# Performance work log

Hardware: AMD Instinct MI355X
Metric: run time of the kernel (lower is better)

Reference implementation:

```python
import jax, jax.numpy as jnp
import numpy as np

N_Q = 24
MEAS = (2, 5, 10, 18, 21)


def _build_gates():
    # encoding layer: RY(edge[i]) on wire i
    g = [("ry", "e", i, i) for i in range(N_Q)]
    spec = [
        ("ry", 0, 0), ("ry", 1, 1), ("cx", 0, 1),
        ("ry", 2, 2), ("ry", 3, 3), ("cx", 3, 2),
        ("ry", 4, 4), ("ry", 5, 5), ("cx", 4, 5),
        ("ry", 6, 6), ("ry", 7, 7), ("cx", 7, 6),
        ("ry", 8, 8), ("ry", 9, 9), ("cx", 8, 9),
        ("ry", 10, 10), ("ry", 11, 11), ("cx", 11, 10),
        ("ry", 12, 12), ("ry", 13, 13), ("cx", 12, 13),
        ("ry", 14, 14), ("ry", 15, 15), ("cx", 15, 14),
        ("ry", 16, 16), ("ry", 17, 17), ("cx", 16, 17),
        ("ry", 18, 18), ("ry", 19, 19), ("cx", 19, 18),
        ("ry", 20, 20), ("ry", 21, 21), ("cx", 20, 21),
        ("ry", 22, 22), ("ry", 23, 23), ("cx", 23, 22),
        ("ry", 24, 1), ("ry", 25, 2), ("cx", 1, 2),
        ("ry", 26, 5), ("ry", 27, 6), ("cx", 6, 5),
        ("ry", 28, 9), ("ry", 29, 10), ("cx", 9, 10),
        ("ry", 30, 13), ("ry", 31, 14), ("cx", 14, 13),
        ("ry", 32, 17), ("ry", 33, 18), ("cx", 17, 18),
        ("ry", 34, 21), ("ry", 35, 22), ("cx", 22, 21),
        ("ry", 36, 2), ("ry", 37, 5), ("cx", 2, 5),
        ("ry", 38, 10), ("ry", 39, 13), ("cx", 13, 10),
        ("ry", 40, 18), ("ry", 41, 21), ("cx", 21, 18),
        ("ry", 42, 5), ("ry", 43, 10), ("cx", 5, 10),
        ("ry", 44, 10), ("ry", 45, 18), ("cx", 10, 18),
        ("ry", 46, 5), ("ry", 47, 10), ("cx", 10, 5),
        ("ry", 48, 18), ("ry", 49, 21), ("cx", 18, 21),
        ("ry", 50, 2), ("ry", 51, 5), ("cx", 5, 2),
        ("ry", 52, 2), ("ry", 53, 5), ("ry", 54, 10), ("ry", 55, 18), ("ry", 56, 21),
    ]
    for op in spec:
        if op[0] == "ry":
            g.append(("ry", "t", op[1], op[2]))
        else:
            g.append(("cx", op[1], op[2]))
    return g


GATES = _build_gates()


def _ry(state, ang, w):
    # RY(ang) = [[cos(a/2), -sin(a/2)], [sin(a/2), cos(a/2)]] (real)
    h = 0.5 * ang
    c, s = jnp.cos(h), jnp.sin(h)
    U = jnp.stack([jnp.stack([c, -s]), jnp.stack([s, c])])
    return jnp.moveaxis(jnp.tensordot(U, state, axes=((1,), (w,))), 0, w)


def _cx(state, c, t):
    s = jnp.moveaxis(state, (c, t), (0, 1))
    s = jnp.stack([s[0], s[1][::-1]])  # flip target where control == 1
    return jnp.moveaxis(s, (0, 1), (c, t))


def _expz(state, w):
    p = jnp.moveaxis(state * state, w, 0)
    return jnp.sum(p[0]) - jnp.sum(p[1])


def _run(edge, theta):
    state = jnp.zeros((2,) * N_Q, jnp.float32).at[(0,) * N_Q].set(1.0)
    for g in GATES:
        if g[0] == "ry":
            ang = edge[g[2]] if g[1] == "e" else theta[g[2]]
            state = _ry(state, ang, g[3])
        else:
            state = _cx(state, g[1], g[2])
    return state


def _node_out(edge, theta):
    st = _run(edge, theta)
    ev = jnp.stack([_expz(st, w) for w in MEAS])
    return jnp.pi * (1.0 - ev)  # 2*pi*(1 - ev)/2


def setup_inputs() -> dict:
    key = jax.random.key(0)
    k0, k1, k2, k3, k4 = jax.random.split(key, 5)
    N, E, D = 4, 16, 8
    X = jax.random.uniform(k0, (N, D), jnp.float32)
    e = jax.random.uniform(k1, (E,), jnp.float32)
    Ri = jax.random.uniform(k2, (N, E), jnp.float32)
    Ro = jax.random.uniform(k3, (N, E), jnp.float32)
    theta = jax.random.uniform(k4, (57,), jnp.float32, 0.0, 2.0 * np.pi)
    return {"X": X, "e": e, "Ri": Ri, "Ro": Ro, "theta": theta}


def reference(X, e, Ri, Ro, theta):
    bo = Ro.T @ X                     # [E, D]
    bi = Ri.T @ X                     # [E, D]
    Rwo = Ro * e                      # edge-weighted incidence, e broadcasts over E
    Rwi = Ri * e
    mi = Rwi @ bo                     # [N, D]
    mo = Rwo @ bi                     # [N, D]
    M = jnp.concatenate([mi, mo, X], axis=1)  # [N, 24] angles per node
    return jax.vmap(_node_out, in_axes=(0, None))(M, theta)  # [N, 5]
```

## Files before the change

### kernel.cpp

```cpp
#include <hip/hip_runtime.h>
#include <math.h>


__device__ __forceinline__ void ry_dm(float& a, float& b, float& d, float c, float s) {
    float na = c*c*a - 2.0f*c*s*b + s*s*d;
    float nb = c*s*(a - d) + (c*c - s*s)*b;
    float nd = s*s*a + 2.0f*c*s*b + c*c*d;
    a = na; b = nb; d = nd;
}

template<int MASK>
__device__ __forceinline__ void apply_ry(float* amp, float c, float s) {
#pragma unroll
    for (int i = 0; i < 32; ++i) {
        if (!(i & MASK)) {
            float x = amp[i], y = amp[i | MASK];
            amp[i]        = c * x - s * y;
            amp[i | MASK] = s * x + c * y;
        }
    }
}

template<int MC, int MT>
__device__ __forceinline__ void apply_cx(float* amp) {
#pragma unroll
    for (int i = 0; i < 32; ++i) {
        if ((i & MC) && !(i & MT)) {
            float tmp = amp[i];
            amp[i] = amp[i | MT];
            amp[i | MT] = tmp;
        }
    }
}

__global__ __launch_bounds__(64) void nodenet_branch_kernel(
    const float* __restrict__ X, const float* __restrict__ e,
    const float* __restrict__ Ri, const float* __restrict__ Ro,
    const float* __restrict__ th, float* __restrict__ out)
{
    const int t    = threadIdx.x;
    const int node = blockIdx.x * 2 + (t >> 5);
    const int lig  = t & 31;
    const int base = t & 32;

    float Mv;
    {
        const int w    = lig & 15;
        const int half = lig >> 4;
        const int dcol = w & 7;
        const float* Aouter = (w < 8) ? Ri : Ro;
        const float* Ainner = (w < 8) ? Ro : Ri;
        const float x0 = X[0*8 + dcol], x1 = X[1*8 + dcol],
                    x2 = X[2*8 + dcol], x3 = X[3*8 + dcol];
        float acc = 0.0f;
        const int E0 = half * 8;
#pragma unroll
        for (int E = 0; E < 8; ++E) {
            const int Ei = E0 + E;
            float bsum = Ainner[0*16 + Ei]*x0 + Ainner[1*16 + Ei]*x1
                       + Ainner[2*16 + Ei]*x2 + Ainner[3*16 + Ei]*x3;
            acc += Aouter[node*16 + Ei] * e[Ei] * bsum;
        }
        acc += __shfl_xor(acc, 16);
        Mv = (lig < 16) ? acc : X[node*8 + ((lig - 16) & 7)];
    }

    float gs, gc;
    {
        const int id = (lig < 21) ? lig : 0;
        __sincosf(0.5f * th[36 + id], &gs, &gc);
    }

    const int ss = (lig < 6) ? lig : 0;
    const int Q   = ss==0?2 : ss==1?5 : ss==2?10 : ss==3?13 : ss==4?18 : 21;
    const int P   = ss==0?3 : ss==1?4 : ss==2?11 : ss==3?12 : ss==4?19 : 20;
    const int C   = ss==0?1 : ss==1?6 : ss==2?9  : ss==3?14 : ss==4?17 : 22;
    const int PC  = ss==0?0 : ss==1?7 : ss==2?8  : ss==3?15 : ss==4?16 : 23;
    const int tq2 = ss==0?25: ss==1?26: ss==2?29 : ss==3?30 : ss==4?33 : 34;
    const int tc2 = ss==0?24: ss==1?27: ss==2?28 : ss==3?31 : ss==4?32 : 35;

    const float mq  = __shfl(Mv, base + Q);
    const float mp  = __shfl(Mv, base + P);
    const float mc  = __shfl(Mv, base + C);
    const float mpc = __shfl(Mv, base + PC);

    float ra, rb, rd;
    {
        float sq, cq, sp, cp;
        __sincosf(0.5f*(mq + th[Q]), &sq, &cq);
        __sincosf(0.5f*(mp + th[P]), &sp, &cp);
        float aq = cp*cp*cq*cq + sp*sp*sq*sq;
        float bq = cq*sq;
        float dq = 1.0f - aq;

        float sc, cc, spc, cpc;
        __sincosf(0.5f*(mc + th[C]), &sc, &cc);
        __sincosf(0.5f*(mpc + th[PC]), &spc, &cpc);
        float ac = cpc*cpc*cc*cc + spc*spc*sc*sc;
        float bc = cc*sc;
        float dc = 1.0f - ac;

        float s2, c2;
        __sincosf(0.5f*th[tc2], &s2, &c2);
        float p0 = c2*c2*ac - 2.0f*c2*s2*bc + s2*s2*dc;

        float s1, c1;
        __sincosf(0.5f*th[tq2], &s1, &c1);
        ry_dm(aq, bq, dq, c1, s1);
        ra = p0*aq + (1.0f - p0)*dq;
        rb = bq;
        rd = p0*dq + (1.0f - p0)*aq;
    }

    {
        const float c38 = __shfl(gc, base + 2), s38 = __shfl(gs, base + 2);
        const float c39 = __shfl(gc, base + 3), s39 = __shfl(gs, base + 3);
        const float a3 = __shfl(ra, base + 3);
        const float b3 = __shfl(rb, base + 3);
        const float d3 = __shfl(rd, base + 3);
        float a = ra, b = rb, d = rd;
        ry_dm(a, b, d, c38, s38);
        float p0 = c39*c39*a3 - 2.0f*c39*s39*b3 + s39*s39*d3;
        float fa = p0*a + (1.0f - p0)*d;
        float fd = p0*d + (1.0f - p0)*a;
        if (lig == 2) { ra = fa; rb = b; rd = fd; }
    }

    float cph, sph, lam0;
    {
        float ad = ra - rd;
        float r  = sqrtf(ad*ad + 4.0f*rb*rb);
        lam0 = 0.5f * (1.0f + r);
        float c2p = (r > 1e-12f) ? ad / r : 1.0f;
        float s2p = (r > 1e-12f) ? 2.0f*rb / r : 0.0f;
        cph = sqrtf(fmaxf(0.0f, 0.5f*(1.0f + c2p)));
        sph = copysignf(sqrtf(fmaxf(0.0f, 0.5f*(1.0f - c2p))), s2p);
    }

    float u0[5], u1[5];
    float wgt = 1.0f;
    {
        const int slotOf[5] = {0, 1, 2, 4, 5};
#pragma unroll
        for (int b = 0; b < 5; ++b) {
            const float cb = __shfl(cph,  base + slotOf[b]);
            const float sb = __shfl(sph,  base + slotOf[b]);
            const float lb = __shfl(lam0, base + slotOf[b]);
            const int bit = (lig >> b) & 1;
            u0[b] = bit ? -sb : cb;
            u1[b] = bit ?  cb : sb;
            wgt  *= bit ? (1.0f - lb) : lb;
        }
    }

    float c_, s_;
#define BC(id) do { c_ = __shfl(gc, base + (id)); s_ = __shfl(gs, base + (id)); } while (0)

    BC(0); float v00 = c_*u0[0] - s_*u1[0], v01 = s_*u0[0] + c_*u1[0];
    BC(1); float v10 = c_*u0[1] - s_*u1[1], v11 = s_*u0[1] + c_*u1[1];
    float q01_0 = v00*v10, q01_1 = v01*v11, q01_2 = v00*v11, q01_3 = v01*v10;

    BC(4); float v30 = c_*u0[3] - s_*u1[3], v31 = s_*u0[3] + c_*u1[3];
    BC(5); float v40 = c_*u0[4] - s_*u1[4], v41 = s_*u0[4] + c_*u1[4];
    float q34_0 = v30*v40, q34_1 = v31*v40, q34_2 = v31*v41, q34_3 = v30*v41;

    BC(6);
    { float x = q01_0, y = q01_2; q01_0 = c_*x - s_*y; q01_2 = s_*x + c_*y;
      x = q01_1; y = q01_3;       q01_1 = c_*x - s_*y; q01_3 = s_*x + c_*y; }
    BC(7); float v20 = c_*u0[2] - s_*u1[2], v21 = s_*u0[2] + c_*u1[2];
    float q012[8];
    q012[0] = q01_0*v20; q012[1] = q01_1*v20; q012[2] = q01_2*v21; q012[3] = q01_3*v21;
    q012[4] = q01_0*v21; q012[5] = q01_1*v21; q012[6] = q01_2*v20; q012[7] = q01_3*v20;

    BC(8);
#pragma unroll
    for (int j = 0; j < 4; ++j) {
        float x = q012[j], y = q012[j + 4];
        q012[j] = c_*x - s_*y; q012[j + 4] = s_*x + c_*y;
    }
    BC(10);
    { float x, y;
      x = q012[0]; y = q012[2]; q012[0] = c_*x - s_*y; q012[2] = s_*x + c_*y;
      x = q012[1]; y = q012[3]; q012[1] = c_*x - s_*y; q012[3] = s_*x + c_*y;
      x = q012[4]; y = q012[6]; q012[4] = c_*x - s_*y; q012[6] = s_*x + c_*y;
      x = q012[5]; y = q012[7]; q012[5] = c_*x - s_*y; q012[7] = s_*x + c_*y; }

    BC(9);
    { float x = q34_0, y = q34_1; q34_0 = c_*x - s_*y; q34_1 = s_*x + c_*y;
      x = q34_2; y = q34_3;       q34_2 = c_*x - s_*y; q34_3 = s_*x + c_*y; }
    BC(13);
    { float x = q34_0, y = q34_2; q34_0 = c_*x - s_*y; q34_2 = s_*x + c_*y;
      x = q34_1; y = q34_3;       q34_1 = c_*x - s_*y; q34_3 = s_*x + c_*y; }

    float q34a[4] = {q34_0, q34_1, q34_2, q34_3};
    float amp[32];
#pragma unroll
    for (int j = 0; j < 32; ++j) {
        const int i2 = (j >> 2) & 1, i3 = (j >> 3) & 1, i4 = (j >> 4) & 1;
        amp[j] = q012[j & 7] * q34a[(i3 ^ i2) + 2*i4];
    }

    BC(11); apply_ry<4>(amp, c_, s_);
    apply_cx<4, 2>(amp);
    BC(12); apply_ry<8>(amp, c_, s_);
    apply_cx<8, 16>(amp);
    BC(14); apply_ry<1>(amp, c_, s_);
    BC(15); apply_ry<2>(amp, c_, s_);
    apply_cx<2, 1>(amp);

    float p[32];
#pragma unroll
    for (int j = 0; j < 32; ++j) p[j] = amp[j] * amp[j];

    float z0 = 0.f, z1 = 0.f, z2 = 0.f, z3 = 0.f, z4;
    float s0[16];
#pragma unroll
    for (int i = 0; i < 16; ++i) { s0[i] = p[2*i] + p[2*i+1]; z0 += p[2*i] - p[2*i+1]; }
    float s1v[8];
#pragma unroll
    for (int i = 0; i < 8; ++i)  { s1v[i] = s0[2*i] + s0[2*i+1]; z1 += s0[2*i] - s0[2*i+1]; }
    float s2v[4];
#pragma unroll
    for (int i = 0; i < 4; ++i)  { s2v[i] = s1v[2*i] + s1v[2*i+1]; z2 += s1v[2*i] - s1v[2*i+1]; }
    float s3v[2];
#pragma unroll
    for (int i = 0; i < 2; ++i)  { s3v[i] = s2v[2*i] + s2v[2*i+1]; z3 += s2v[2*i] - s2v[2*i+1]; }
    z4 = s3v[0] - s3v[1];
    const float zv[5] = {z0, z1, z2, z3, z4};

    float xv[5];
#pragma unroll
    for (int b = 0; b < 5; ++b) {
        const int m = 1 << b;
        float acc = 0.0f;
#pragma unroll
        for (int i = 0; i < 32; ++i)
            if (!(i & m)) acc += amp[i] * amp[i | m];
        xv[b] = 2.0f * acc;
    }

    float ev[5];
#pragma unroll
    for (int b = 0; b < 5; ++b) {
        BC(16 + b);
        ev[b] = wgt * ((c_*c_ - s_*s_) * zv[b] - 2.0f*c_*s_ * xv[b]);
    }
#undef BC

#pragma unroll
    for (int off = 1; off < 32; off <<= 1) {
#pragma unroll
        for (int b = 0; b < 5; ++b) ev[b] += __shfl_xor(ev[b], off);
    }

    if (lig < 5) {
        const float v = lig==0 ? ev[0] : lig==1 ? ev[1] : lig==2 ? ev[2]
                      : lig==3 ? ev[3] : ev[4];
        out[node*5 + lig] = 3.14159265358979f * (1.0f - v);
    }
}

extern "C" void kernel_launch(void* const* d_in, const int* in_sizes, int n_in,
                              void* d_out, int out_size, void* d_ws, size_t ws_size,
                              hipStream_t stream) {
    const float* X  = (const float*)d_in[0];
    const float* e  = (const float*)d_in[1];
    const float* Ri = (const float*)d_in[2];
    const float* Ro = (const float*)d_in[3];
    const float* th = (const float*)d_in[4];
    float* out = (float*)d_out;

    nodenet_branch_kernel<<<2, 64, 0, stream>>>(X, e, Ri, Ro, th, out);
}
```

Measured before the change: 9.585 us.

## Split each node's 32-amplitude state across two half-wavefronts, one node per block

Each node now gets a full 64-lane block, and the qubit-4 index is distributed across the two 32-lane halves. Every lane holds 16 amplitudes instead of 32. Gates that touch that bit become cross-half shuffles, and the launch grows from 2 to 4 blocks. The aim is to halve the per-thread serial arithmetic and register pressure on this latency-bound kernel, at the cost of extra cross-lane shuffles and a longer reduction.

```diff
diff --git a/kernel.cpp b/kernel.cpp
--- a/kernel.cpp
+++ b/kernel.cpp
@@ -10,25 +10,13 @@
 }
 
 template<int MASK>
-__device__ __forceinline__ void apply_ry(float* amp, float c, float s) {
-#pragma unroll
-    for (int i = 0; i < 32; ++i) {
+__device__ __forceinline__ void apply_ry16(float* amp, float c, float s) {
+#pragma unroll
+    for (int i = 0; i < 16; ++i) {
         if (!(i & MASK)) {
             float x = amp[i], y = amp[i | MASK];
             amp[i]        = c * x - s * y;
             amp[i | MASK] = s * x + c * y;
-        }
-    }
-}
-
-template<int MC, int MT>
-__device__ __forceinline__ void apply_cx(float* amp) {
-#pragma unroll
-    for (int i = 0; i < 32; ++i) {
-        if ((i & MC) && !(i & MT)) {
-            float tmp = amp[i];
-            amp[i] = amp[i | MT];
-            amp[i | MT] = tmp;
         }
     }
 }
@@ -39,17 +27,16 @@
     const float* __restrict__ th, float* __restrict__ out)
 {
     const int t    = threadIdx.x;
-    const int node = blockIdx.x * 2 + (t >> 5);
+    const int node = blockIdx.x;
     const int lig  = t & 31;
-    const int base = t & 32;
+    const int half = t >> 5;
 
     float Mv;
     {
-        const int w    = lig & 15;
-        const int half = lig >> 4;
+        const int w    = lig;
         const int dcol = w & 7;
-        const float* Aouter = (w < 8) ? Ri : Ro;
-        const float* Ainner = (w < 8) ? Ro : Ri;
+        const float* Aouter = ((w & 8) == 0) ? Ri : Ro;
+        const float* Ainner = ((w & 8) == 0) ? Ro : Ri;
         const float x0 = X[0*8 + dcol], x1 = X[1*8 + dcol],
                     x2 = X[2*8 + dcol], x3 = X[3*8 + dcol];
         float acc = 0.0f;
@@ -61,7 +48,7 @@
                        + Ainner[2*16 + Ei]*x2 + Ainner[3*16 + Ei]*x3;
             acc += Aouter[node*16 + Ei] * e[Ei] * bsum;
         }
-        acc += __shfl_xor(acc, 16);
+        acc += __shfl_xor(acc, 32);
         Mv = (lig < 16) ? acc : X[node*8 + ((lig - 16) & 7)];
     }
 
@@ -79,10 +66,10 @@
     const int tq2 = ss==0?25: ss==1?26: ss==2?29 : ss==3?30 : ss==4?33 : 34;
     const int tc2 = ss==0?24: ss==1?27: ss==2?28 : ss==3?31 : ss==4?32 : 35;
 
-    const float mq  = __shfl(Mv, base + Q);
-    const float mp  = __shfl(Mv, base + P);
-    const float mc  = __shfl(Mv, base + C);
-    const float mpc = __shfl(Mv, base + PC);
+    const float mq  = __shfl(Mv, Q);
+    const float mp  = __shfl(Mv, P);
+    const float mc  = __shfl(Mv, C);
+    const float mpc = __shfl(Mv, PC);
 
     float ra, rb, rd;
     {
@@ -113,11 +100,11 @@
     }
 
     {
-        const float c38 = __shfl(gc, base + 2), s38 = __shfl(gs, base + 2);
-        const float c39 = __shfl(gc, base + 3), s39 = __shfl(gs, base + 3);
-        const float a3 = __shfl(ra, base + 3);
-        const float b3 = __shfl(rb, base + 3);
-        const float d3 = __shfl(rd, base + 3);
+        const float c38 = __shfl(gc, 2), s38 = __shfl(gs, 2);
+        const float c39 = __shfl(gc, 3), s39 = __shfl(gs, 3);
+        const float a3 = __shfl(ra, 3);
+        const float b3 = __shfl(rb, 3);
+        const float d3 = __shfl(rd, 3);
         float a = ra, b = rb, d = rd;
         ry_dm(a, b, d, c38, s38);
         float p0 = c39*c39*a3 - 2.0f*c39*s39*b3 + s39*s39*d3;
@@ -143,9 +130,9 @@
         const int slotOf[5] = {0, 1, 2, 4, 5};
 #pragma unroll
         for (int b = 0; b < 5; ++b) {
-            const float cb = __shfl(cph,  base + slotOf[b]);
-            const float sb = __shfl(sph,  base + slotOf[b]);
-            const float lb = __shfl(lam0, base + slotOf[b]);
+            const float cb = __shfl(cph,  slotOf[b]);
+            const float sb = __shfl(sph,  slotOf[b]);
+            const float lb = __shfl(lam0, slotOf[b]);
             const int bit = (lig >> b) & 1;
             u0[b] = bit ? -sb : cb;
             u1[b] = bit ?  cb : sb;
@@ -154,15 +141,11 @@
     }
 
     float c_, s_;
-#define BC(id) do { c_ = __shfl(gc, base + (id)); s_ = __shfl(gs, base + (id)); } while (0)
+#define BC(id) do { c_ = __shfl(gc, (id)); s_ = __shfl(gs, (id)); } while (0)
 
     BC(0); float v00 = c_*u0[0] - s_*u1[0], v01 = s_*u0[0] + c_*u1[0];
     BC(1); float v10 = c_*u0[1] - s_*u1[1], v11 = s_*u0[1] + c_*u1[1];
     float q01_0 = v00*v10, q01_1 = v01*v11, q01_2 = v00*v11, q01_3 = v01*v10;
-
-    BC(4); float v30 = c_*u0[3] - s_*u1[3], v31 = s_*u0[3] + c_*u1[3];
-    BC(5); float v40 = c_*u0[4] - s_*u1[4], v41 = s_*u0[4] + c_*u1[4];
-    float q34_0 = v30*v40, q34_1 = v31*v40, q34_2 = v31*v41, q34_3 = v30*v41;
 
     BC(6);
     { float x = q01_0, y = q01_2; q01_0 = c_*x - s_*y; q01_2 = s_*x + c_*y;
@@ -184,59 +167,85 @@
       x = q012[1]; y = q012[3]; q012[1] = c_*x - s_*y; q012[3] = s_*x + c_*y;
       x = q012[4]; y = q012[6]; q012[4] = c_*x - s_*y; q012[6] = s_*x + c_*y;
       x = q012[5]; y = q012[7]; q012[5] = c_*x - s_*y; q012[7] = s_*x + c_*y; }
-
+    BC(14);
+    { float x, y;
+      x = q012[0]; y = q012[1]; q012[0] = c_*x - s_*y; q012[1] = s_*x + c_*y;
+      x = q012[2]; y = q012[3]; q012[2] = c_*x - s_*y; q012[3] = s_*x + c_*y;
+      x = q012[4]; y = q012[5]; q012[4] = c_*x - s_*y; q012[5] = s_*x + c_*y;
+      x = q012[6]; y = q012[7]; q012[6] = c_*x - s_*y; q012[7] = s_*x + c_*y; }
+
+    BC(4); float v30 = c_*u0[3] - s_*u1[3], v31 = s_*u0[3] + c_*u1[3];
+    BC(5); float v4h = half ? (s_*u0[4] + c_*u1[4]) : (c_*u0[4] - s_*u1[4]);
+    float qA = (half ? v31 : v30) * v4h;
+    float qB = (half ? v30 : v31) * v4h;
     BC(9);
-    { float x = q34_0, y = q34_1; q34_0 = c_*x - s_*y; q34_1 = s_*x + c_*y;
-      x = q34_2; y = q34_3;       q34_2 = c_*x - s_*y; q34_3 = s_*x + c_*y; }
+    { float x = qA, y = qB; qA = c_*x - s_*y; qB = s_*x + c_*y; }
     BC(13);
-    { float x = q34_0, y = q34_2; q34_0 = c_*x - s_*y; q34_2 = s_*x + c_*y;
-      x = q34_1; y = q34_3;       q34_1 = c_*x - s_*y; q34_3 = s_*x + c_*y; }
-
-    float q34a[4] = {q34_0, q34_1, q34_2, q34_3};
-    float amp[32];
-#pragma unroll
-    for (int j = 0; j < 32; ++j) {
-        const int i2 = (j >> 2) & 1, i3 = (j >> 3) & 1, i4 = (j >> 4) & 1;
-        amp[j] = q012[j & 7] * q34a[(i3 ^ i2) + 2*i4];
-    }
-
-    BC(11); apply_ry<4>(amp, c_, s_);
-    apply_cx<4, 2>(amp);
-    BC(12); apply_ry<8>(amp, c_, s_);
-    apply_cx<8, 16>(amp);
-    BC(14); apply_ry<1>(amp, c_, s_);
-    BC(15); apply_ry<2>(amp, c_, s_);
-    apply_cx<2, 1>(amp);
-
-    float p[32];
-#pragma unroll
-    for (int j = 0; j < 32; ++j) p[j] = amp[j] * amp[j];
-
-    float z0 = 0.f, z1 = 0.f, z2 = 0.f, z3 = 0.f, z4;
-    float s0[16];
-#pragma unroll
-    for (int i = 0; i < 16; ++i) { s0[i] = p[2*i] + p[2*i+1]; z0 += p[2*i] - p[2*i+1]; }
-    float s1v[8];
-#pragma unroll
-    for (int i = 0; i < 8; ++i)  { s1v[i] = s0[2*i] + s0[2*i+1]; z1 += s0[2*i] - s0[2*i+1]; }
-    float s2v[4];
-#pragma unroll
-    for (int i = 0; i < 4; ++i)  { s2v[i] = s1v[2*i] + s1v[2*i+1]; z2 += s1v[2*i] - s1v[2*i+1]; }
-    float s3v[2];
-#pragma unroll
-    for (int i = 0; i < 2; ++i)  { s3v[i] = s2v[2*i] + s2v[2*i+1]; z3 += s2v[2*i] - s2v[2*i+1]; }
-    z4 = s3v[0] - s3v[1];
+    {
+        const float oA = __shfl_xor(qA, 32);
+        const float oB = __shfl_xor(qB, 32);
+        const float sgn = half ? s_ : -s_;
+        qA = c_*qA + sgn*oA;
+        qB = c_*qB + sgn*oB;
+    }
+
+    float amp[16];
+#pragma unroll
+    for (int j = 0; j < 16; ++j) {
+        const int sel = ((j >> 3) ^ (j >> 2)) & 1;
+        amp[j] = q012[j & 7] * (sel ? qB : qA);
+    }
+
+    BC(11); apply_ry16<4>(amp, c_, s_);
+    { float tmp;
+      tmp = amp[4];  amp[4]  = amp[6];  amp[6]  = tmp;
+      tmp = amp[5];  amp[5]  = amp[7];  amp[7]  = tmp;
+      tmp = amp[12]; amp[12] = amp[14]; amp[14] = tmp;
+      tmp = amp[13]; amp[13] = amp[15]; amp[15] = tmp; }
+    BC(12); apply_ry16<8>(amp, c_, s_);
+#pragma unroll
+    for (int j = 8; j < 16; ++j) amp[j] = __shfl_xor(amp[j], 32);
+    BC(15); apply_ry16<2>(amp, c_, s_);
+    { float tmp;
+      tmp = amp[2];  amp[2]  = amp[3];  amp[3]  = tmp;
+      tmp = amp[6];  amp[6]  = amp[7];  amp[7]  = tmp;
+      tmp = amp[10]; amp[10] = amp[11]; amp[11] = tmp;
+      tmp = amp[14]; amp[14] = amp[15]; amp[15] = tmp; }
+
+    float p[16];
+#pragma unroll
+    for (int j = 0; j < 16; ++j) p[j] = amp[j] * amp[j];
+
+    float z0 = 0.f, z1 = 0.f, z2 = 0.f, z3, z4;
+    float s0[8];
+#pragma unroll
+    for (int i = 0; i < 8; ++i) { s0[i] = p[2*i] + p[2*i+1]; z0 += p[2*i] - p[2*i+1]; }
+    float s1v[4];
+#pragma unroll
+    for (int i = 0; i < 4; ++i) { s1v[i] = s0[2*i] + s0[2*i+1]; z1 += s0[2*i] - s0[2*i+1]; }
+    float s2v[2];
+#pragma unroll
+    for (int i = 0; i < 2; ++i) { s2v[i] = s1v[2*i] + s1v[2*i+1]; z2 += s1v[2*i] - s1v[2*i+1]; }
+    z3 = s2v[0] - s2v[1];
+    const float tot = s2v[0] + s2v[1];
+    z4 = half ? -tot : tot;
     const float zv[5] = {z0, z1, z2, z3, z4};
 
     float xv[5];
 #pragma unroll
-    for (int b = 0; b < 5; ++b) {
+    for (int b = 0; b < 4; ++b) {
         const int m = 1 << b;
         float acc = 0.0f;
 #pragma unroll
-        for (int i = 0; i < 32; ++i)
-            if (!(i & m)) acc += amp[i] * amp[i | m];
+        for (int j = 0; j < 16; ++j)
+            if (!(j & m)) acc += amp[j] * amp[j | m];
         xv[b] = 2.0f * acc;
+    }
+    {
+        float acc = 0.0f;
+#pragma unroll
+        for (int j = 0; j < 16; ++j) acc += amp[j] * __shfl_xor(amp[j], 32);
+        xv[4] = acc;
     }
 
     float ev[5];
@@ -248,15 +257,15 @@
 #undef BC
 
 #pragma unroll
-    for (int off = 1; off < 32; off <<= 1) {
+    for (int off = 1; off < 64; off <<= 1) {
 #pragma unroll
         for (int b = 0; b < 5; ++b) ev[b] += __shfl_xor(ev[b], off);
     }
 
-    if (lig < 5) {
-        const float v = lig==0 ? ev[0] : lig==1 ? ev[1] : lig==2 ? ev[2]
-                      : lig==3 ? ev[3] : ev[4];
-        out[node*5 + lig] = 3.14159265358979f * (1.0f - v);
+    if (t < 5) {
+        const float v = t==0 ? ev[0] : t==1 ? ev[1] : t==2 ? ev[2]
+                      : t==3 ? ev[3] : ev[4];
+        out[node*5 + t] = 3.14159265358979f * (1.0f - v);
     }
 }
 
@@ -270,5 +279,5 @@
     const float* th = (const float*)d_in[4];
     float* out = (float*)d_out;
 
-    nodenet_branch_kernel<<<2, 64, 0, stream>>>(X, e, Ri, Ro, th, out);
-}
+    nodenet_branch_kernel<<<4, 64, 0, stream>>>(X, e, Ri, Ro, th, out);
+}
```

Measured after the change: 9.678 us. No clear change (+1.0%).
